# Kernel tuning notes

Hardware: AMD Instinct MI355X
Metric: run time of the kernel (lower is better)

Reference implementation:

```python
import math
import jax, jax.numpy as jnp
import numpy as np

EMBED = 1024
HEADS = 16
DEPTH = 12
HEAD_DIM = EMBED // HEADS // 2  # 32
LAMBDA_INIT = 0.8 - 0.6 * math.exp(-0.3 * DEPTH)


def setup_inputs() -> dict:
    key = jax.random.key(0)
    ks = jax.random.split(key, 11)
    B, T, S = 2, 2048, 2048
    std = 1.0 / math.sqrt(EMBED)
    return {
        "query_x": jax.random.normal(ks[0], (B, T, EMBED), jnp.float32),
        "kv_x": jax.random.normal(ks[1], (B, S, EMBED), jnp.float32),
        "Wq": jax.random.normal(ks[2], (EMBED, EMBED), jnp.float32) * std,
        "Wk": jax.random.normal(ks[3], (EMBED, EMBED), jnp.float32) * std,
        "Wv": jax.random.normal(ks[4], (EMBED, EMBED), jnp.float32) * std,
        "Wo": jax.random.normal(ks[5], (EMBED, EMBED), jnp.float32) * std,
        "lambda_q1": jax.random.normal(ks[6], (HEAD_DIM,), jnp.float32) * 0.1,
        "lambda_k1": jax.random.normal(ks[7], (HEAD_DIM,), jnp.float32) * 0.1,
        "lambda_q2": jax.random.normal(ks[8], (HEAD_DIM,), jnp.float32) * 0.1,
        "lambda_k2": jax.random.normal(ks[9], (HEAD_DIM,), jnp.float32) * 0.1,
        "subln_w": jnp.ones((2 * HEAD_DIM,), jnp.float32),
    }


def rms_norm(x, w, eps=1e-5):
    xf = x.astype(jnp.float32)
    out = xf * jax.lax.rsqrt(jnp.mean(xf * xf, axis=-1, keepdims=True) + eps)
    return out.astype(x.dtype) * w


def reference(query_x, kv_x, Wq, Wk, Wv, Wo, lambda_q1, lambda_k1, lambda_q2, lambda_k2, subln_w):
    B, T, _ = query_x.shape
    S = kv_x.shape[1]
    H, D = HEADS, HEAD_DIM
    scaling = D ** -0.5

    q = (query_x @ Wq).reshape(B, T, 2 * H, D).transpose(0, 2, 1, 3)  # [B,2H,T,D]
    k = (kv_x @ Wk).reshape(B, S, 2 * H, D).transpose(0, 2, 1, 3)     # [B,2H,S,D]
    v = (kv_x @ Wv).reshape(B, S, H, 2 * D).transpose(0, 2, 1, 3)     # [B,H,S,2D]

    scores = jnp.einsum("bhtd,bhsd->bhts", q * scaling, k)            # [B,2H,T,S]
    attn_w = jax.nn.softmax(scores.astype(jnp.float32), axis=-1).astype(scores.dtype)

    lambda_1 = jnp.exp(jnp.sum(lambda_q1 * lambda_k1).astype(jnp.float32))
    lambda_2 = jnp.exp(jnp.sum(lambda_q2 * lambda_k2).astype(jnp.float32))
    lambda_full = (lambda_1 - lambda_2 + LAMBDA_INIT).astype(q.dtype)

    attn_w = attn_w.reshape(B, H, 2, T, S)
    attn_w = attn_w[:, :, 0] - lambda_full * attn_w[:, :, 1]          # [B,H,T,S]

    attn = jnp.einsum("bhts,bhse->bhte", attn_w, v)                   # [B,H,T,2D]
    attn = rms_norm(attn, subln_w) * (1.0 - LAMBDA_INIT)
    attn = attn.transpose(0, 2, 1, 3).reshape(B, T, H * 2 * D)
    return attn @ Wo
```

## Files before the change

kernel.cpp:

```cpp
#include <hip/hip_runtime.h>
#include <stdint.h>


#define LAMBDA_INIT_F 0.7836057665316245f
#define OUT_SCALE_F   0.2163942334683755f
#define QK_SCALE_F    0.17677669529663687f
#define LOG2E_F       1.4426950408889634f

typedef _Float16 f16x8 __attribute__((ext_vector_type(8)));
typedef _Float16 f16x4 __attribute__((ext_vector_type(4)));
typedef _Float16 f16x2 __attribute__((ext_vector_type(2)));
typedef __fp16   h16x2 __attribute__((ext_vector_type(2)));
typedef float    f32x4 __attribute__((ext_vector_type(4)));
typedef float    f32x16 __attribute__((ext_vector_type(16)));

__device__ inline void gl_lds16(const void* g, void* l) {
  __builtin_amdgcn_global_load_lds(
      (const __attribute__((address_space(1))) void*)g,
      (__attribute__((address_space(3))) void*)l, 16, 0, 0);
}

__device__ inline f16x2 cvtpk(float a, float b) {
  h16x2 r = __builtin_amdgcn_cvt_pkrtz(a, b);
  return __builtin_bit_cast(f16x2, r);
}

__global__ __launch_bounds__(256) void prep(
    const float* __restrict__ qx, const float* __restrict__ kvx,
    const float* __restrict__ Wq, const float* __restrict__ Wk,
    const float* __restrict__ Wv, const float* __restrict__ Wo,
    const float* __restrict__ lq1, const float* __restrict__ lk1,
    const float* __restrict__ lq2, const float* __restrict__ lk2,
    _Float16* __restrict__ xq, _Float16* __restrict__ xkv,
    _Float16* __restrict__ WqT, _Float16* __restrict__ WkT,
    _Float16* __restrict__ WvT, _Float16* __restrict__ WoT,
    float* __restrict__ lamv) {
  __shared__ _Float16 t[64][65];
  const int bb = blockIdx.x;
  const int tid = threadIdx.x;
  if (bb < 8192) {
    const float* src = (bb < 4096) ? qx : kvx;
    _Float16* dst = (bb < 4096) ? xq : xkv;
    int i = ((bb & 4095) * 256 + tid) * 4;
    float4 v = *(const float4*)(src + i);
    f16x4 o;
    o[0] = (_Float16)v.x; o[1] = (_Float16)v.y;
    o[2] = (_Float16)v.z; o[3] = (_Float16)v.w;
    *(f16x4*)(dst + i) = o;
  } else if (bb < 9216) {
    const int idx = bb - 8192;
    const int w = idx >> 8, loc = idx & 255;
    const float* W = (w == 0) ? Wq : (w == 1) ? Wk : (w == 2) ? Wv : Wo;
    _Float16* Wt   = (w == 0) ? WqT : (w == 1) ? WkT : (w == 2) ? WvT : WoT;
    const float scale = (w == 0) ? QK_SCALE_F * LOG2E_F : 1.0f;
    const int nb = (loc & 15) * 64, kb2 = (loc >> 4) * 64;
#pragma unroll
    for (int p = 0; p < 16; ++p) {
      int i = p * 256 + tid;
      int r = i >> 6, c = i & 63;
      t[c][r] = (_Float16)(W[(size_t)(kb2 + r) * 1024 + nb + c] * scale);
    }
    __syncthreads();
#pragma unroll
    for (int p = 0; p < 16; ++p) {
      int i = p * 256 + tid;
      int r = i >> 6, c = i & 63;
      Wt[(size_t)(nb + r) * 1024 + kb2 + c] = t[r][c];
    }
  } else {
    if (tid < 64) {
      int l = tid;
      float a = (l < 32) ? lq1[l] * lk1[l] : 0.f;
      float b = (l < 32) ? lq2[l] * lk2[l] : 0.f;
#pragma unroll
      for (int m = 1; m < 64; m <<= 1) {
        a += __shfl_xor(a, m, 64);
        b += __shfl_xor(b, m, 64);
      }
      if (l == 0) lamv[0] = expf(a) - expf(b) + LAMBDA_INIT_F;
    }
  }
}

__global__ __launch_bounds__(256, 4) void gemmseg(
    const _Float16* __restrict__ A0, const _Float16* __restrict__ B0, _Float16* __restrict__ C0,
    const _Float16* __restrict__ A1, const _Float16* __restrict__ B1, _Float16* __restrict__ C1,
    const _Float16* __restrict__ A2, const _Float16* __restrict__ B2, _Float16* __restrict__ C2,
    int nseg, float* __restrict__ Cf32) {
  __shared__ alignas(16) _Float16 As[2][4096];
  __shared__ alignas(16) _Float16 Bs[2][4096];
  const int tid = threadIdx.x;
  const int lane = tid & 63, wid = tid >> 6;
  const int g = lane >> 4, ln = lane & 15;
  const int wm = wid >> 1, wn = wid & 1;

  const int nwg = nseg << 8;
  const int b0 = blockIdx.x;
  const int swz = (b0 & 7) * (nwg >> 3) + (b0 >> 3);
  const int seg = swz >> 8, loc = swz & 255;
  const _Float16 *A, *B;
  _Float16* C;
  if (seg == 0)      { A = A0; B = B0; C = C0; }
  else if (seg == 1) { A = A1; B = B1; C = C1; }
  else               { A = A2; B = B2; C = C2; }
  int bm, bn, N;
  if (seg == 2) { N = 4096; bm = (loc >> 5) << 7; bn = (loc & 31) << 7; }
  else          { N = 1024; bm = (loc >> 3) << 7; bn = (loc & 7) << 7; }
  const int K = 1024;

  f32x4 acc[4][4];
#pragma unroll
  for (int i = 0; i < 4; ++i)
#pragma unroll
    for (int j = 0; j < 4; ++j) acc[i][j] = (f32x4){0.f, 0.f, 0.f, 0.f};

  int aoff[4], boff[4];
#pragma unroll
  for (int i = 0; i < 4; ++i) {
    int r = wm * 64 + i * 16 + ln;
    aoff[i] = r * 32 + (((g + ((r >> 1) & 3)) & 3) << 3);
    r = wn * 64 + i * 16 + ln;
    boff[i] = r * 32 + (((g + ((r >> 1) & 3)) & 3) << 3);
  }

  auto STAGE = [&](int buf, int kt) {
#pragma unroll
    for (int l2 = 0; l2 < 2; ++l2) {
      int ci = l2 * 256 + wid * 64 + lane;
      int r = ci >> 2, cp = ci & 3;
      int c = (cp - ((r >> 1) & 3)) & 3;
      gl_lds16(A + (size_t)(bm + r) * K + kt + c * 8,
               (void*)&As[buf][l2 * 2048 + wid * 512]);
      gl_lds16(B + (size_t)(bn + r) * K + kt + c * 8,
               (void*)&Bs[buf][l2 * 2048 + wid * 512]);
    }
  };

  STAGE(0, 0);
  __syncthreads();
  int buf = 0;
  for (int kt = 0; kt < K; kt += 32) {
    if (kt + 32 < K) STAGE(buf ^ 1, kt + 32);
    f16x8 af[4], bf[4];
#pragma unroll
    for (int i = 0; i < 4; ++i) {
      af[i] = *(const f16x8*)(&As[buf][aoff[i]]);
      bf[i] = *(const f16x8*)(&Bs[buf][boff[i]]);
    }
#pragma unroll
    for (int i = 0; i < 4; ++i)
#pragma unroll
      for (int j = 0; j < 4; ++j)
        acc[i][j] = __builtin_amdgcn_mfma_f32_16x16x32_f16(af[i], bf[j], acc[i][j], 0, 0, 0);
    __syncthreads();
    buf ^= 1;
  }

#pragma unroll
  for (int i = 0; i < 4; ++i) {
#pragma unroll
    for (int j = 0; j < 4; ++j) {
      int grow = bm + wm * 64 + i * 16 + g * 4;
      int gcol = bn + wn * 64 + j * 16 + ln;
#pragma unroll
      for (int r = 0; r < 4; ++r) {
        if (Cf32) Cf32[(size_t)(grow + r) * N + gcol] = acc[i][j][r];
        else      C[(size_t)(grow + r) * N + gcol] = (_Float16)acc[i][j][r];
      }
    }
  }
}

__global__ __launch_bounds__(512, 2) void diffattn(const _Float16* __restrict__ qb,
                                                   const _Float16* __restrict__ kb,
                                                   const _Float16* __restrict__ vT,
                                                   const float* __restrict__ lam_p,
                                                   const float* __restrict__ subw,
                                                   _Float16* __restrict__ attn16) {
  __shared__ alignas(16) _Float16 stg[2][8192];

  const int tid = threadIdx.x;
  const int lane = tid & 63, wid = tid >> 6;
  const int q32 = lane & 31;
  const int hl = lane >> 5;
  const int wq = wid & 1;
  const int comp = (wid >> 1) & 1;
  const int sh = wid >> 2;
  const int bid = blockIdx.x;
  const int wg = ((bid & 7) << 6) | (bid >> 3);
  const int qt = wg & 15;
  const int h = (wg >> 4) & 15;
  const int b = wg >> 8;
  const int trowA = qt * 128 + wq * 64 + q32;

  const _Float16* qpA = qb + ((size_t)b * 2048 + trowA) * 1024 + (2 * h + comp) * 32 + hl * 8;
  f16x8 qfA0 = *(const f16x8*)(qpA);
  f16x8 qfA1 = *(const f16x8*)(qpA + 16);
  const _Float16* qpB = qpA + (size_t)32 * 1024;
  f16x8 qfB0 = *(const f16x8*)(qpB);
  f16x8 qfB1 = *(const f16x8*)(qpB + 16);

  const _Float16* kg;
  {
    const int r = (wid & 1) * 16 + (lane >> 2);
    const int pos = lane & 3;
    const int c = (pos - ((r >> 1) & 3)) & 3;
    kg = kb + ((size_t)b * 2048 + (size_t)(wid >> 2) * 1024 + r) * 1024 +
         (2 * h + ((wid >> 1) & 1)) * 32 + c * 8;
  }
  const _Float16* vg;
  {
    const int e = wid * 8 + (lane >> 3);
    const int pos = lane & 7;
    const int ca = (pos - (e & 7)) & 7;
    vg = vT + ((size_t)(h * 64 + e)) * 4096 + (size_t)b * 2048 +
         (ca >> 2) * 1024 + (ca & 3) * 8;
  }

  const int kreg = (sh * 2 + comp) * 1024;
  const int sk = (q32 >> 1) & 3;
  const int ko0 = kreg + q32 * 32 + ((hl + sk) & 3) * 8;
  const int ko1 = kreg + q32 * 32 + ((2 + hl + sk) & 3) * 8;
  const int e7 = q32 & 7;
  const int vb0 = 4096 + q32 * 64 + hl * 4;
  const int vp0 = ((sh * 4 + 0 + e7) & 7) * 8;
  const int vp1 = ((sh * 4 + 1 + e7) & 7) * 8;
  const int vp2 = ((sh * 4 + 2 + e7) & 7) * 8;
  const int vp3 = ((sh * 4 + 3 + e7) & 7) * 8;

  f32x16 OA[2] = {}, OB[2] = {};
  float lpA = 0.f, lpB = 0.f;
  const f32x16 zf = {};

  auto STAGE = [&](int buf, int it) {
    gl_lds16(kg + (size_t)it * 32768, (void*)&stg[buf][wid * 512]);
    gl_lds16(vg + it * 32,            (void*)&stg[buf][4096 + wid * 512]);
  };

  auto PROC = [&](int buf) {
    const _Float16* sb = &stg[buf][0];
    f16x8 Kf0 = *(const f16x8*)(sb + ko0);
    f16x8 Kf1 = *(const f16x8*)(sb + ko1);

    __builtin_amdgcn_s_setprio(1);
    f32x16 stA = __builtin_amdgcn_mfma_f32_32x32x16_f16(Kf0, qfA0, zf, 0, 0, 0);
    stA = __builtin_amdgcn_mfma_f32_32x32x16_f16(Kf1, qfA1, stA, 0, 0, 0);
    f32x16 stB = __builtin_amdgcn_mfma_f32_32x32x16_f16(Kf0, qfB0, zf, 0, 0, 0);
    stB = __builtin_amdgcn_mfma_f32_32x32x16_f16(Kf1, qfB1, stB, 0, 0, 0);
    __builtin_amdgcn_s_setprio(0);

    float pA[16], pB[16];
#pragma unroll
    for (int i = 0; i < 16; ++i) pA[i] = __builtin_amdgcn_exp2f(stA[i]);
#pragma unroll
    for (int i = 0; i < 16; ++i) pB[i] = __builtin_amdgcn_exp2f(stB[i]);
    {
      float s8[8];
#pragma unroll
      for (int i = 0; i < 8; ++i) s8[i] = pA[2 * i] + pA[2 * i + 1];
#pragma unroll
      for (int i = 0; i < 4; ++i) s8[i] += s8[i + 4];
      lpA += (s8[0] + s8[1]) + (s8[2] + s8[3]);
    }
    {
      float s8[8];
#pragma unroll
      for (int i = 0; i < 8; ++i) s8[i] = pB[2 * i] + pB[2 * i + 1];
#pragma unroll
      for (int i = 0; i < 4; ++i) s8[i] += s8[i + 4];
      lpB += (s8[0] + s8[1]) + (s8[2] + s8[3]);
    }

    union { f16x8 v; f16x2 h2[4]; } pbA0, pbA1, pbB0, pbB1;
    pbA0.h2[0] = cvtpk(pA[0], pA[1]);   pbA0.h2[1] = cvtpk(pA[2], pA[3]);
    pbA0.h2[2] = cvtpk(pA[4], pA[5]);   pbA0.h2[3] = cvtpk(pA[6], pA[7]);
    pbA1.h2[0] = cvtpk(pA[8], pA[9]);   pbA1.h2[1] = cvtpk(pA[10], pA[11]);
    pbA1.h2[2] = cvtpk(pA[12], pA[13]); pbA1.h2[3] = cvtpk(pA[14], pA[15]);
    pbB0.h2[0] = cvtpk(pB[0], pB[1]);   pbB0.h2[1] = cvtpk(pB[2], pB[3]);
    pbB0.h2[2] = cvtpk(pB[4], pB[5]);   pbB0.h2[3] = cvtpk(pB[6], pB[7]);
    pbB1.h2[0] = cvtpk(pB[8], pB[9]);   pbB1.h2[1] = cvtpk(pB[10], pB[11]);
    pbB1.h2[2] = cvtpk(pB[12], pB[13]); pbB1.h2[3] = cvtpk(pB[14], pB[15]);

    const _Float16* v0 = sb + vb0;
    const _Float16* v1 = sb + vb0 + 2048;
    union { f16x8 v; f16x4 h4[2]; } va0, va1;

    va0.h4[0] = *(const f16x4*)(v0 + vp0); va0.h4[1] = *(const f16x4*)(v0 + vp1);
    va1.h4[0] = *(const f16x4*)(v1 + vp0); va1.h4[1] = *(const f16x4*)(v1 + vp1);
    __builtin_amdgcn_s_setprio(1);
    OA[0] = __builtin_amdgcn_mfma_f32_32x32x16_f16(va0.v, pbA0.v, OA[0], 0, 0, 0);
    OA[1] = __builtin_amdgcn_mfma_f32_32x32x16_f16(va1.v, pbA0.v, OA[1], 0, 0, 0);
    OB[0] = __builtin_amdgcn_mfma_f32_32x32x16_f16(va0.v, pbB0.v, OB[0], 0, 0, 0);
    OB[1] = __builtin_amdgcn_mfma_f32_32x32x16_f16(va1.v, pbB0.v, OB[1], 0, 0, 0);
    __builtin_amdgcn_s_setprio(0);

    va0.h4[0] = *(const f16x4*)(v0 + vp2); va0.h4[1] = *(const f16x4*)(v0 + vp3);
    va1.h4[0] = *(const f16x4*)(v1 + vp2); va1.h4[1] = *(const f16x4*)(v1 + vp3);
    __builtin_amdgcn_s_setprio(1);
    OA[0] = __builtin_amdgcn_mfma_f32_32x32x16_f16(va0.v, pbA1.v, OA[0], 0, 0, 0);
    OA[1] = __builtin_amdgcn_mfma_f32_32x32x16_f16(va1.v, pbA1.v, OA[1], 0, 0, 0);
    OB[0] = __builtin_amdgcn_mfma_f32_32x32x16_f16(va0.v, pbB1.v, OB[0], 0, 0, 0);
    OB[1] = __builtin_amdgcn_mfma_f32_32x32x16_f16(va1.v, pbB1.v, OB[1], 0, 0, 0);
    __builtin_amdgcn_s_setprio(0);
  };

  STAGE(0, 0);
  __syncthreads();
  int buf = 0;
  for (int it = 0; it < 32; ++it) {
    if (it + 1 < 32) STAGE(buf ^ 1, it + 1);
    PROC(buf);
    __syncthreads();
    buf ^= 1;
  }

  float lA = lpA + __shfl_xor(lpA, 32, 64);
  float lB = lpB + __shfl_xor(lpB, 32, 64);

  float* pay = (float*)&stg[0][0];
  _Float16* o2s = (_Float16*)(pay + 2 * 64 * 34);
  const float lam = lam_p[0];

  if (comp == 1 && sh == 1) {
    float* d = pay + (wq * 64 + lane) * 34;
#pragma unroll
    for (int t2 = 0; t2 < 2; ++t2)
#pragma unroll
      for (int i = 0; i < 16; ++i) d[t2 * 16 + i] = OA[t2][i];
    d[32] = lA;
  }
  __syncthreads();
  if (comp == 1 && sh == 0) {
    const float* d = pay + (wq * 64 + lane) * 34;
    lA += d[32];
#pragma unroll
    for (int t2 = 0; t2 < 2; ++t2)
#pragma unroll
      for (int i = 0; i < 16; ++i) OA[t2][i] += d[t2 * 16 + i];
  }
  __syncthreads();
  if (comp == 0 && sh == 1) {
    float* d = pay + (wq * 64 + lane) * 34;
#pragma unroll
    for (int t2 = 0; t2 < 2; ++t2)
#pragma unroll
      for (int i = 0; i < 16; ++i) d[t2 * 16 + i] = OA[t2][i];
    d[32] = lA;
  }
  if (comp == 1 && sh == 0) {
    float rl = 1.f / lA;
    _Float16* d = o2s + (wq * 64 + lane) * 32;
#pragma unroll
    for (int t2 = 0; t2 < 2; ++t2)
#pragma unroll
      for (int i = 0; i < 16; ++i) d[t2 * 16 + i] = (_Float16)(OA[t2][i] * rl);
  }
  __syncthreads();
  if (comp == 0 && sh == 0) {
    const float* d = pay + (wq * 64 + lane) * 34;
    lA += d[32];
#pragma unroll
    for (int t2 = 0; t2 < 2; ++t2)
#pragma unroll
      for (int i = 0; i < 16; ++i) OA[t2][i] += d[t2 * 16 + i];

    const _Float16* d2 = o2s + (wq * 64 + lane) * 32;
    float rl = 1.f / lA;
    float x[2][16];
    float ssq = 0.f;
#pragma unroll
    for (int et = 0; et < 2; ++et)
#pragma unroll
      for (int i = 0; i < 16; ++i) {
        float v = OA[et][i] * rl - lam * (float)d2[et * 16 + i];
        x[et][i] = v;
        ssq += v * v;
      }
    ssq += __shfl_xor(ssq, 32, 64);
    float rms = rsqrtf(ssq * (1.f / 64.f) + 1e-5f) * OUT_SCALE_F;

    _Float16* orow = attn16 + ((size_t)b * 2048 + trowA) * 1024 + h * 64;
#pragma unroll
    for (int et = 0; et < 2; ++et)
#pragma unroll
      for (int grp = 0; grp < 4; ++grp) {
        int e0 = et * 32 + grp * 8 + 4 * hl;
        float4 w = *(const float4*)(subw + e0);
        f16x4 o;
        o[0] = (_Float16)(x[et][grp * 4 + 0] * rms * w.x);
        o[1] = (_Float16)(x[et][grp * 4 + 1] * rms * w.y);
        o[2] = (_Float16)(x[et][grp * 4 + 2] * rms * w.z);
        o[3] = (_Float16)(x[et][grp * 4 + 3] * rms * w.w);
        *(f16x4*)(orow + e0) = o;
      }
  }
  __syncthreads();

  if (comp == 1 && sh == 1) {
    float* d = pay + (wq * 64 + lane) * 34;
#pragma unroll
    for (int t2 = 0; t2 < 2; ++t2)
#pragma unroll
      for (int i = 0; i < 16; ++i) d[t2 * 16 + i] = OB[t2][i];
    d[32] = lB;
  }
  __syncthreads();
  if (comp == 1 && sh == 0) {
    const float* d = pay + (wq * 64 + lane) * 34;
    lB += d[32];
#pragma unroll
    for (int t2 = 0; t2 < 2; ++t2)
#pragma unroll
      for (int i = 0; i < 16; ++i) OB[t2][i] += d[t2 * 16 + i];
  }
  __syncthreads();
  if (comp == 0 && sh == 1) {
    float* d = pay + (wq * 64 + lane) * 34;
#pragma unroll
    for (int t2 = 0; t2 < 2; ++t2)
#pragma unroll
      for (int i = 0; i < 16; ++i) d[t2 * 16 + i] = OB[t2][i];
    d[32] = lB;
  }
  if (comp == 1 && sh == 0) {
    float rl = 1.f / lB;
    _Float16* d = o2s + (wq * 64 + lane) * 32;
#pragma unroll
    for (int t2 = 0; t2 < 2; ++t2)
#pragma unroll
      for (int i = 0; i < 16; ++i) d[t2 * 16 + i] = (_Float16)(OB[t2][i] * rl);
  }
  __syncthreads();
  if (comp == 0 && sh == 0) {
    const float* d = pay + (wq * 64 + lane) * 34;
    lB += d[32];
#pragma unroll
    for (int t2 = 0; t2 < 2; ++t2)
#pragma unroll
      for (int i = 0; i < 16; ++i) OB[t2][i] += d[t2 * 16 + i];

    const _Float16* d2 = o2s + (wq * 64 + lane) * 32;
    float rl = 1.f / lB;
    float x[2][16];
    float ssq = 0.f;
#pragma unroll
    for (int et = 0; et < 2; ++et)
#pragma unroll
      for (int i = 0; i < 16; ++i) {
        float v = OB[et][i] * rl - lam * (float)d2[et * 16 + i];
        x[et][i] = v;
        ssq += v * v;
      }
    ssq += __shfl_xor(ssq, 32, 64);
    float rms = rsqrtf(ssq * (1.f / 64.f) + 1e-5f) * OUT_SCALE_F;

    _Float16* orow = attn16 + ((size_t)b * 2048 + trowA + 32) * 1024 + h * 64;
#pragma unroll
    for (int et = 0; et < 2; ++et)
#pragma unroll
      for (int grp = 0; grp < 4; ++grp) {
        int e0 = et * 32 + grp * 8 + 4 * hl;
        float4 w = *(const float4*)(subw + e0);
        f16x4 o;
        o[0] = (_Float16)(x[et][grp * 4 + 0] * rms * w.x);
        o[1] = (_Float16)(x[et][grp * 4 + 1] * rms * w.y);
        o[2] = (_Float16)(x[et][grp * 4 + 2] * rms * w.z);
        o[3] = (_Float16)(x[et][grp * 4 + 3] * rms * w.w);
        *(f16x4*)(orow + e0) = o;
      }
  }
}

extern "C" void kernel_launch(void* const* d_in, const int* in_sizes, int n_in,
                              void* d_out, int out_size, void* d_ws, size_t ws_size,
                              hipStream_t stream) {
  const float* query_x = (const float*)d_in[0];
  const float* kv_x    = (const float*)d_in[1];
  const float* Wq      = (const float*)d_in[2];
  const float* Wk      = (const float*)d_in[3];
  const float* Wv      = (const float*)d_in[4];
  const float* Wo      = (const float*)d_in[5];
  const float* lq1     = (const float*)d_in[6];
  const float* lk1     = (const float*)d_in[7];
  const float* lq2     = (const float*)d_in[8];
  const float* lk2     = (const float*)d_in[9];
  const float* subw    = (const float*)d_in[10];
  float* out = (float*)d_out;

  const size_t NX = (size_t)4096 * 1024;
  const size_t NW = (size_t)1024 * 1024;
  _Float16* xq  = (_Float16*)d_ws;
  _Float16* xkv = xq  + NX;
  _Float16* WqT = xkv + NX;
  _Float16* WkT = WqT + NW;
  _Float16* WvT = WkT + NW;
  _Float16* WoT = WvT + NW;
  _Float16* qb  = WoT + NW;
  _Float16* kbf = qb  + NX;
  _Float16* vTb = kbf + NX;
  _Float16* a16 = vTb + NX;
  float* lamv   = (float*)(a16 + NX);

  prep<<<9217, 256, 0, stream>>>(query_x, kv_x, Wq, Wk, Wv, Wo,
                                 lq1, lk1, lq2, lk2,
                                 xq, xkv, WqT, WkT, WvT, WoT, lamv);

  gemmseg<<<768, 256, 0, stream>>>(xq, WqT, qb,
                                   xkv, WkT, kbf,
                                   WvT, xkv, vTb,
                                   3, nullptr);

  diffattn<<<512, 512, 0, stream>>>(qb, kbf, vTb, lamv, subw, a16);

  gemmseg<<<256, 256, 0, stream>>>(a16, WoT, nullptr,
                                   nullptr, nullptr, nullptr,
                                   nullptr, nullptr, nullptr,
                                   1, out);
}
```

Before: 147.7 us.

## Split attention blocks into 256-thread workgroups covering 64 query rows

The attention kernel now launches 1024 workgroups of 4 waves, each covering 64 query rows, instead of 512 workgroups of 8 waves covering 128 rows. Each wave issues twice as many global-to-LDS staging loads so the same K/V tile still fills shared memory. The aim is finer-grained scheduling and cheaper block-wide barriers. In exchange, each K/V tile is reused by half as many query rows, so total K/V load traffic doubles.

```diff
diff --git a/kernel.cpp b/kernel.cpp
--- a/kernel.cpp
+++ b/kernel.cpp
@@ -171,7 +171,7 @@
   }
 }
 
-__global__ __launch_bounds__(512, 2) void diffattn(const _Float16* __restrict__ qb,
+__global__ __launch_bounds__(256, 4) void diffattn(const _Float16* __restrict__ qb,
                                                    const _Float16* __restrict__ kb,
                                                    const _Float16* __restrict__ vT,
                                                    const float* __restrict__ lam_p,
@@ -183,15 +183,14 @@
   const int lane = tid & 63, wid = tid >> 6;
   const int q32 = lane & 31;
   const int hl = lane >> 5;
-  const int wq = wid & 1;
-  const int comp = (wid >> 1) & 1;
-  const int sh = wid >> 2;
+  const int comp = wid & 1;
+  const int sh = wid >> 1;
   const int bid = blockIdx.x;
-  const int wg = ((bid & 7) << 6) | (bid >> 3);
-  const int qt = wg & 15;
-  const int h = (wg >> 4) & 15;
-  const int b = wg >> 8;
-  const int trowA = qt * 128 + wq * 64 + q32;
+  const int wg = ((bid & 7) << 7) | (bid >> 3);
+  const int qt = wg & 31;
+  const int h = (wg >> 5) & 15;
+  const int b = wg >> 9;
+  const int trowA = qt * 64 + q32;
 
   const _Float16* qpA = qb + ((size_t)b * 2048 + trowA) * 1024 + (2 * h + comp) * 32 + hl * 8;
   f16x8 qfA0 = *(const f16x8*)(qpA);
@@ -200,21 +199,28 @@
   f16x8 qfB0 = *(const f16x8*)(qpB);
   f16x8 qfB1 = *(const f16x8*)(qpB + 16);
 
-  const _Float16* kg;
+  const _Float16 *kg0, *kg1;
   {
-    const int r = (wid & 1) * 16 + (lane >> 2);
-    const int pos = lane & 3;
-    const int c = (pos - ((r >> 1) & 3)) & 3;
-    kg = kb + ((size_t)b * 2048 + (size_t)(wid >> 2) * 1024 + r) * 1024 +
-         (2 * h + ((wid >> 1) & 1)) * 32 + c * 8;
-  }
-  const _Float16* vg;
+    const int r0 = (lane >> 2);
+    const int c0 = ((lane & 3) - ((r0 >> 1) & 3)) & 3;
+    kg0 = kb + ((size_t)b * 2048 + (size_t)sh * 1024 + r0) * 1024 +
+          (2 * h + comp) * 32 + c0 * 8;
+    const int r1 = 16 + (lane >> 2);
+    const int c1 = ((lane & 3) - ((r1 >> 1) & 3)) & 3;
+    kg1 = kb + ((size_t)b * 2048 + (size_t)sh * 1024 + r1) * 1024 +
+          (2 * h + comp) * 32 + c1 * 8;
+  }
+  const _Float16 *vg0, *vg1;
   {
-    const int e = wid * 8 + (lane >> 3);
     const int pos = lane & 7;
-    const int ca = (pos - (e & 7)) & 7;
-    vg = vT + ((size_t)(h * 64 + e)) * 4096 + (size_t)b * 2048 +
-         (ca >> 2) * 1024 + (ca & 3) * 8;
+    const int e0 = wid * 16 + (lane >> 3);
+    const int ca0 = (pos - (e0 & 7)) & 7;
+    vg0 = vT + ((size_t)(h * 64 + e0)) * 4096 + (size_t)b * 2048 +
+          (ca0 >> 2) * 1024 + (ca0 & 3) * 8;
+    const int e1 = e0 + 8;
+    const int ca1 = (pos - (e1 & 7)) & 7;
+    vg1 = vT + ((size_t)(h * 64 + e1)) * 4096 + (size_t)b * 2048 +
+          (ca1 >> 2) * 1024 + (ca1 & 3) * 8;
   }
 
   const int kreg = (sh * 2 + comp) * 1024;
@@ -233,8 +239,10 @@
   const f32x16 zf = {};
 
   auto STAGE = [&](int buf, int it) {
-    gl_lds16(kg + (size_t)it * 32768, (void*)&stg[buf][wid * 512]);
-    gl_lds16(vg + it * 32,            (void*)&stg[buf][4096 + wid * 512]);
+    gl_lds16(kg0 + (size_t)it * 32768, (void*)&stg[buf][wid * 1024]);
+    gl_lds16(kg1 + (size_t)it * 32768, (void*)&stg[buf][wid * 1024 + 512]);
+    gl_lds16(vg0 + it * 32,            (void*)&stg[buf][4096 + wid * 1024]);
+    gl_lds16(vg1 + it * 32,            (void*)&stg[buf][4096 + wid * 1024 + 512]);
   };
 
   auto PROC = [&](int buf) {
@@ -318,11 +326,11 @@
   float lB = lpB + __shfl_xor(lpB, 32, 64);
 
   float* pay = (float*)&stg[0][0];
-  _Float16* o2s = (_Float16*)(pay + 2 * 64 * 34);
+  _Float16* o2s = (_Float16*)(pay + 64 * 34);
   const float lam = lam_p[0];
 
   if (comp == 1 && sh == 1) {
-    float* d = pay + (wq * 64 + lane) * 34;
+    float* d = pay + lane * 34;
 #pragma unroll
     for (int t2 = 0; t2 < 2; ++t2)
 #pragma unroll
@@ -331,7 +339,7 @@
   }
   __syncthreads();
   if (comp == 1 && sh == 0) {
-    const float* d = pay + (wq * 64 + lane) * 34;
+    const float* d = pay + lane * 34;
     lA += d[32];
 #pragma unroll
     for (int t2 = 0; t2 < 2; ++t2)
@@ -340,7 +348,7 @@
   }
   __syncthreads();
   if (comp == 0 && sh == 1) {
-    float* d = pay + (wq * 64 + lane) * 34;
+    float* d = pay + lane * 34;
 #pragma unroll
     for (int t2 = 0; t2 < 2; ++t2)
 #pragma unroll
@@ -349,7 +357,7 @@
   }
   if (comp == 1 && sh == 0) {
     float rl = 1.f / lA;
-    _Float16* d = o2s + (wq * 64 + lane) * 32;
+    _Float16* d = o2s + lane * 32;
 #pragma unroll
     for (int t2 = 0; t2 < 2; ++t2)
 #pragma unroll
@@ -357,14 +365,14 @@
   }
   __syncthreads();
   if (comp == 0 && sh == 0) {
-    const float* d = pay + (wq * 64 + lane) * 34;
+    const float* d = pay + lane * 34;
     lA += d[32];
 #pragma unroll
     for (int t2 = 0; t2 < 2; ++t2)
 #pragma unroll
       for (int i = 0; i < 16; ++i) OA[t2][i] += d[t2 * 16 + i];
 
-    const _Float16* d2 = o2s + (wq * 64 + lane) * 32;
+    const _Float16* d2 = o2s + lane * 32;
     float rl = 1.f / lA;
     float x[2][16];
     float ssq = 0.f;
@@ -397,7 +405,7 @@
   __syncthreads();
 
   if (comp == 1 && sh == 1) {
-    float* d = pay + (wq * 64 + lane) * 34;
+    float* d = pay + lane * 34;
 #pragma unroll
     for (int t2 = 0; t2 < 2; ++t2)
 #pragma unroll
@@ -406,7 +414,7 @@
   }
   __syncthreads();
   if (comp == 1 && sh == 0) {
-    const float* d = pay + (wq * 64 + lane) * 34;
+    const float* d = pay + lane * 34;
     lB += d[32];
 #pragma unroll
     for (int t2 = 0; t2 < 2; ++t2)
@@ -415,7 +423,7 @@
   }
   __syncthreads();
   if (comp == 0 && sh == 1) {
-    float* d = pay + (wq * 64 + lane) * 34;
+    float* d = pay + lane * 34;
 #pragma unroll
     for (int t2 = 0; t2 < 2; ++t2)
 #pragma unroll
@@ -424,7 +432,7 @@
   }
   if (comp == 1 && sh == 0) {
     float rl = 1.f / lB;
-    _Float16* d = o2s + (wq * 64 + lane) * 32;
+    _Float16* d = o2s + lane * 32;
 #pragma unroll
     for (int t2 = 0; t2 < 2; ++t2)
 #pragma unroll
@@ -432,14 +440,14 @@
   }
   __syncthreads();
   if (comp == 0 && sh == 0) {
-    const float* d = pay + (wq * 64 + lane) * 34;
+    const float* d = pay + lane * 34;
     lB += d[32];
 #pragma unroll
     for (int t2 = 0; t2 < 2; ++t2)
 #pragma unroll
       for (int i = 0; i < 16; ++i) OB[t2][i] += d[t2 * 16 + i];
 
-    const _Float16* d2 = o2s + (wq * 64 + lane) * 32;
+    const _Float16* d2 = o2s + lane * 32;
     float rl = 1.f / lB;
     float x[2][16];
     float ssq = 0.f;
@@ -510,7 +518,7 @@
                                    WvT, xkv, vTb,
                                    3, nullptr);
 
-  diffattn<<<512, 512, 0, stream>>>(qb, kbf, vTb, lamv, subw, a16);
+  diffattn<<<1024, 256, 0, stream>>>(qb, kbf, vTb, lamv, subw, a16);
 
   gemmseg<<<256, 256, 0, stream>>>(a16, WoT, nullptr,
                                    nullptr, nullptr, nullptr,
```

New measurement: 309.0 us. +109.1%, slower.
